# Performance work log

Measured on AMD Instinct MI355X. Metric: run time of the kernel, lower is better.

Reference implementation:

```python
import jax, jax.numpy as jnp
import numpy as np

NGRAMS = 5


def _pair_idx():
    pairs = [(i, j) for i in range(NGRAMS) for j in range(i + 1, NGRAMS)]
    return (np.array([p[0] for p in pairs]), np.array([p[1] for p in pairs]))


def setup_inputs() -> dict:
    key = jax.random.key(0)
    ks = jax.random.split(key, 12)
    B, S, U = 8, 500, 128
    n = NGRAMS
    C = S // n          # 100 chunks
    F = n * (n - 1)     # 2 * C(n,2) = 20 edge-concat feature width
    H, DK = n, 2        # per-chunk MHA: 5 heads, key_dim=value_dim=2
    GH, GD = 4, U // 4  # graph MHA: 4 heads, key_dim=32
    s = 0.05
    inp = {
        'x': jax.random.normal(ks[0], (B, S, U), jnp.float32),
        'wq': s * jax.random.normal(ks[1], (C, F, H, DK), jnp.float32),
        'bq': jnp.zeros((C, H, DK), jnp.float32),
        'wk': s * jax.random.normal(ks[2], (C, F, H, DK), jnp.float32),
        'bk': jnp.zeros((C, H, DK), jnp.float32),
        'wv': s * jax.random.normal(ks[3], (C, F, H, DK), jnp.float32),
        'bv': jnp.zeros((C, H, DK), jnp.float32),
        'wo': s * jax.random.normal(ks[4], (C, H, DK, F), jnp.float32),
        'bo': jnp.zeros((C, F), jnp.float32),
        'pos': 0.02 * jax.random.normal(ks[5], (C, U), jnp.float32),
        'gwq': s * jax.random.normal(ks[6], (U, GH, GD), jnp.float32),
        'gbq': jnp.zeros((GH, GD), jnp.float32),
        'gwk': s * jax.random.normal(ks[7], (U, GH, GD), jnp.float32),
        'gbk': jnp.zeros((GH, GD), jnp.float32),
        'gwv': s * jax.random.normal(ks[8], (U, GH, GD), jnp.float32),
        'gbv': jnp.zeros((GH, GD), jnp.float32),
        'gwo': s * jax.random.normal(ks[9], (GH, GD, U), jnp.float32),
        'gbo': jnp.zeros((U,), jnp.float32),
    }
    return inp


def reference(x, wq, bq, wk, bk, wv, bv, wo, bo, pos,
              gwq, gbq, gwk, gbk, gwv, gbv, gwo, gbo):
    B, S, U = x.shape
    n = NGRAMS
    C = S // n
    ii, jj = _pair_idx()
    P = ii.shape[0]
    # [B,S,U] -> [B,U,S] -> chunks [B,U,C,n]
    xt = jnp.transpose(x, (0, 2, 1)).reshape(B, U, C, n)
    # edge construction: concat of every node pair per chunk -> [B,U,C,2P]
    H_edges = jnp.stack([xt[..., ii], xt[..., jj]], axis=-1).reshape(B, U, C, 2 * P)
    Ht = jnp.transpose(H_edges, (0, 2, 1, 3))  # [B,C,U,F], attention seq axis = U
    dk = wq.shape[-1]
    scale = 1.0 / jnp.sqrt(jnp.asarray(dk, x.dtype))
    q = (jnp.einsum('bcuf,cfhd->bcuhd', Ht, wq) + bq[None, :, None]) * scale
    k = jnp.einsum('bcuf,cfhd->bcuhd', Ht, wk) + bk[None, :, None]
    v = jnp.einsum('bcuf,cfhd->bcuhd', Ht, wv) + bv[None, :, None]
    scores = jnp.einsum('bcuhd,bcvhd->bchuv', q, k)
    attn = jax.nn.softmax(scores, axis=-1)
    o = jnp.einsum('bchuv,bcvhd->bcuhd', attn, v)
    mha_out = jnp.einsum('bcuhd,chdf->bcuf', o, wo) + bo[None, :, None]
    alpha = jax.nn.leaky_relu(Ht + mha_out, negative_slope=0.3)  # [B,C,U,F]
    # stack + reduce_mean over edge-feature axis, transpose -> [B,C,U]
    g = jnp.mean(alpha, axis=-1)
    g = g + pos[None]  # learned position embedding over C
    # graph-level self-attention over the C axis
    gdk = gwq.shape[-1]
    gscale = 1.0 / jnp.sqrt(jnp.asarray(gdk, x.dtype))
    gq = (jnp.einsum('bcu,uhd->bchd', g, gwq) + gbq) * gscale
    gk = jnp.einsum('bcu,uhd->bchd', g, gwk) + gbk
    gv = jnp.einsum('bcu,uhd->bchd', g, gwv) + gbv
    gs = jnp.einsum('bqhd,bkhd->bhqk', gq, gk)
    ga = jax.nn.softmax(gs, axis=-1)
    go = jnp.einsum('bhqk,bkhd->bqhd', ga, gv)
    g_attn = jnp.einsum('bqhd,hdu->bqu', go, gwo) + gbo
    return g + g_attn  # [B, C, U]
```

## Files before the change

kernel.cpp:

```cpp
#include <hip/hip_runtime.h>

#define NB  8
#define SS  500
#define UU  128
#define NG  5
#define CC  100
#define PP  10
#define FF  20
#define HH  5
#define HD  10
#define GHH 4
#define GDD 32

__global__ __launch_bounds__(128) void k1_chunk_mha(
    const float* __restrict__ x,   const float* __restrict__ wq,
    const float* __restrict__ bq,  const float* __restrict__ wk,
    const float* __restrict__ bk,  const float* __restrict__ wv,
    const float* __restrict__ bv,  const float* __restrict__ wo,
    const float* __restrict__ bo,  const float* __restrict__ pos,
    const float* __restrict__ gwq, const float* __restrict__ gbq,
    const float* __restrict__ gwk, const float* __restrict__ gbk,
    const float* __restrict__ gwv, const float* __restrict__ gbv,
    float* __restrict__ g_out, float* __restrict__ gq_out,
    float* __restrict__ gk_out, float* __restrict__ gv_out)
{
    const int bc = blockIdx.x;
    const int b  = bc / CC, c = bc % CC;
    const int u  = threadIdx.x;

    __shared__ float4 s_kv[UU][HH];
    __shared__ float  s_g[UU];

    float xv[NG];
    const float* xb = x + (size_t)b * SS * UU + (size_t)c * NG * UU + u;
#pragma unroll
    for (int t = 0; t < NG; ++t) xv[t] = xb[t * UU];

    const int II[PP] = {0,0,0,0,1,1,1,2,2,3};
    const int JJ[PP] = {1,2,3,4,2,3,4,3,4,4};
    float ht[FF];
#pragma unroll
    for (int p = 0; p < PP; ++p) { ht[2*p] = xv[II[p]]; ht[2*p+1] = xv[JJ[p]]; }

    const float* wqc = wq + c * (FF * HD);
    const float* wkc = wk + c * (FF * HD);
    const float* wvc = wv + c * (FF * HD);
    float qv[HD], kv[HD], vv[HD];
#pragma unroll
    for (int hd = 0; hd < HD; ++hd) {
        qv[hd] = bq[c*HD + hd]; kv[hd] = bk[c*HD + hd]; vv[hd] = bv[c*HD + hd];
    }
#pragma unroll
    for (int f = 0; f < FF; ++f) {
        const float hf = ht[f];
#pragma unroll
        for (int hd = 0; hd < HD; ++hd) {
            qv[hd] = fmaf(hf, wqc[f*HD + hd], qv[hd]);
            kv[hd] = fmaf(hf, wkc[f*HD + hd], kv[hd]);
            vv[hd] = fmaf(hf, wvc[f*HD + hd], vv[hd]);
        }
    }
#pragma unroll
    for (int h = 0; h < HH; ++h)
        s_kv[u][h] = make_float4(kv[2*h], kv[2*h+1], vv[2*h], vv[2*h+1]);
    __syncthreads();

    const float scale = 0.7071067811865476f;
    float q0[HH], q1[HH], l[HH], o0[HH], o1[HH];
#pragma unroll
    for (int h = 0; h < HH; ++h) {
        q0[h] = qv[2*h] * scale; q1[h] = qv[2*h+1] * scale;
        l[h] = 0.f; o0[h] = 0.f; o1[h] = 0.f;
    }
#pragma unroll 2
    for (int vi = 0; vi < UU; ++vi) {
#pragma unroll
        for (int h = 0; h < HH; ++h) {
            const float4 kvv = s_kv[vi][h];
            const float s = fmaf(q0[h], kvv.x, q1[h] * kvv.y);
            const float e = __expf(s);
            l[h]  += e;
            o0[h]  = fmaf(e, kvv.z, o0[h]);
            o1[h]  = fmaf(e, kvv.w, o1[h]);
        }
    }
    float o[HD];
#pragma unroll
    for (int h = 0; h < HH; ++h) {
        const float inv = 1.f / l[h];
        o[2*h] = o0[h] * inv; o[2*h+1] = o1[h] * inv;
    }

    const float* woc = wo + c * (HD * FF);
    float gsum = 0.f;
#pragma unroll
    for (int f = 0; f < FF; ++f) {
        float acc = bo[c*FF + f];
#pragma unroll
        for (int hd = 0; hd < HD; ++hd) acc = fmaf(o[hd], woc[hd*FF + f], acc);
        const float a = ht[f] + acc;
        gsum += (a > 0.f) ? a : 0.3f * a;
    }
    const float g = gsum * (1.f / FF) + pos[c*UU + u];
    g_out[(size_t)bc*UU + u] = g;
    s_g[u] = g;
    __syncthreads();

    const float gscale = 0.17677669529663687f;
    float aq = gbq[u], ak = gbk[u], av = gbv[u];
    for (int u2 = 0; u2 < UU; ++u2) {
        const float gu = s_g[u2];
        aq = fmaf(gu, gwq[u2*UU + u], aq);
        ak = fmaf(gu, gwk[u2*UU + u], ak);
        av = fmaf(gu, gwv[u2*UU + u], av);
    }
    gq_out[(size_t)bc*UU + u] = aq * gscale;
    gk_out[(size_t)bc*UU + u] = ak;
    gv_out[(size_t)bc*UU + u] = av;
}

__global__ __launch_bounds__(128) void k2_graph_attn(
    const float* gq, const float* __restrict__ gk,
    const float* __restrict__ gv, float* go)
{
    const int b = blockIdx.x / GHH, h = blockIdx.x % GHH;
    const int t = threadIdx.x;
    __shared__ float4 s_k[CC][GDD/4], s_v[CC][GDD/4];

    const float4* gk4 = (const float4*)(gk + (size_t)b * CC * UU);
    const float4* gv4 = (const float4*)(gv + (size_t)b * CC * UU);
    for (int idx = t; idx < CC * 8; idx += 128) {
        const int k = idx >> 3, d4 = idx & 7;
        s_k[k][d4] = gk4[k*32 + h*8 + d4];
        s_v[k][d4] = gv4[k*32 + h*8 + d4];
    }
    float4 qf[8];
    if (t < CC) {
        const float4* q4 = (const float4*)(gq + (size_t)b*CC*UU + (size_t)t*UU + h*GDD);
#pragma unroll
        for (int i = 0; i < 8; ++i) qf[i] = q4[i];
    }
    __syncthreads();

    if (t < CC) {
        float l = 0.f;
        float4 o[8];
#pragma unroll
        for (int i = 0; i < 8; ++i) o[i] = make_float4(0.f, 0.f, 0.f, 0.f);
        for (int k = 0; k < CC; ++k) {
            float s = 0.f;
#pragma unroll
            for (int i = 0; i < 8; ++i) {
                const float4 kf = s_k[k][i];
                s = fmaf(qf[i].x, kf.x, s); s = fmaf(qf[i].y, kf.y, s);
                s = fmaf(qf[i].z, kf.z, s); s = fmaf(qf[i].w, kf.w, s);
            }
            const float e = __expf(s);
            l += e;
#pragma unroll
            for (int i = 0; i < 8; ++i) {
                const float4 vf = s_v[k][i];
                o[i].x = fmaf(e, vf.x, o[i].x); o[i].y = fmaf(e, vf.y, o[i].y);
                o[i].z = fmaf(e, vf.z, o[i].z); o[i].w = fmaf(e, vf.w, o[i].w);
            }
        }
        const float inv = 1.f / l;
        float4* go4 = (float4*)(go + (size_t)b*CC*UU + (size_t)t*UU + h*GDD);
#pragma unroll
        for (int i = 0; i < 8; ++i) {
            o[i].x *= inv; o[i].y *= inv; o[i].z *= inv; o[i].w *= inv;
            go4[i] = o[i];
        }
    }
}

__global__ __launch_bounds__(128) void k3_out(
    const float* __restrict__ go, const float* __restrict__ gwo,
    const float* __restrict__ gbo, float* out)
{
    const int bq = blockIdx.x;
    const int u  = threadIdx.x;
    __shared__ float s_go[UU];
    s_go[u] = go[(size_t)bq*UU + u];
    __syncthreads();
    float acc = gbo[u];
    for (int hd = 0; hd < UU; ++hd)
        acc = fmaf(s_go[hd], gwo[hd*UU + u], acc);
    out[(size_t)bq*UU + u] += acc;
}

extern "C" void kernel_launch(void* const* d_in, const int* in_sizes, int n_in,
                              void* d_out, int out_size, void* d_ws, size_t ws_size,
                              hipStream_t stream)
{
    (void)in_sizes; (void)n_in; (void)out_size; (void)ws_size;
    const float* x   = (const float*)d_in[0];
    const float* wq  = (const float*)d_in[1];
    const float* bq  = (const float*)d_in[2];
    const float* wk  = (const float*)d_in[3];
    const float* bk  = (const float*)d_in[4];
    const float* wv  = (const float*)d_in[5];
    const float* bv  = (const float*)d_in[6];
    const float* wo  = (const float*)d_in[7];
    const float* bo  = (const float*)d_in[8];
    const float* pos = (const float*)d_in[9];
    const float* gwq = (const float*)d_in[10];
    const float* gbq = (const float*)d_in[11];
    const float* gwk = (const float*)d_in[12];
    const float* gbk = (const float*)d_in[13];
    const float* gwv = (const float*)d_in[14];
    const float* gbv = (const float*)d_in[15];
    const float* gwo = (const float*)d_in[16];
    const float* gbo = (const float*)d_in[17];
    float* out = (float*)d_out;
    float* ws  = (float*)d_ws;

    float* gq_ws = ws;
    float* gk_ws = ws + 102400;
    float* gv_ws = ws + 204800;

    k1_chunk_mha<<<NB*CC, 128, 0, stream>>>(x, wq, bq, wk, bk, wv, bv, wo, bo,
        pos, gwq, gbq, gwk, gbk, gwv, gbv, out, gq_ws, gk_ws, gv_ws);
    k2_graph_attn<<<NB*GHH, 128, 0, stream>>>(gq_ws, gk_ws, gv_ws, gq_ws);
    k3_out<<<NB*CC, 128, 0, stream>>>(gq_ws, gwo, gbo, out);
}
```

Measured before the change: 145.9 us.

## Split chunk MHA across heads and fuse graph attention with output projection

The chunk kernel now runs 640 threads per block, one group of 128 per head, instead of one thread looping over all five heads. The per-chunk projection and graph QKV work is split across these groups and combined with shared-memory reductions. The graph attention and output projection kernels merge into one kernel with a block per (batch, query). That block recomputes scores over all keys and reads V straight from global memory. This adds parallelism to the serial softmax loop and the small k2 grid, and removes one launch, at the cost of extra syncs and repeated K/V reads per query.

```diff
diff --git a/kernel.cpp b/kernel.cpp
--- a/kernel.cpp
+++ b/kernel.cpp
@@ -12,7 +12,7 @@
 #define GHH 4
 #define GDD 32
 
-__global__ __launch_bounds__(128) void k1_chunk_mha(
+__global__ __launch_bounds__(640) void k1_chunk_mha(
     const float* __restrict__ x,   const float* __restrict__ wq,
     const float* __restrict__ bq,  const float* __restrict__ wk,
     const float* __restrict__ bk,  const float* __restrict__ wv,
@@ -26,10 +26,14 @@
 {
     const int bc = blockIdx.x;
     const int b  = bc / CC, c = bc % CC;
-    const int u  = threadIdx.x;
+    const int u  = threadIdx.x & 127;
+    const int h  = threadIdx.x >> 7;
 
     __shared__ float4 s_kv[UU][HH];
+    __shared__ float2 s_o[UU][HH];
+    __shared__ float  s_part[HH][UU];
     __shared__ float  s_g[UU];
+    __shared__ float  s_red[3][HH][UU];
 
     float xv[NG];
     const float* xb = x + (size_t)b * SS * UU + (size_t)c * NG * UU + u;
@@ -42,151 +46,144 @@
 #pragma unroll
     for (int p = 0; p < PP; ++p) { ht[2*p] = xv[II[p]]; ht[2*p+1] = xv[JJ[p]]; }
 
-    const float* wqc = wq + c * (FF * HD);
-    const float* wkc = wk + c * (FF * HD);
-    const float* wvc = wv + c * (FF * HD);
-    float qv[HD], kv[HD], vv[HD];
-#pragma unroll
-    for (int hd = 0; hd < HD; ++hd) {
-        qv[hd] = bq[c*HD + hd]; kv[hd] = bk[c*HD + hd]; vv[hd] = bv[c*HD + hd];
-    }
+    const int cb = c * (FF * HD) + 2 * h;
+    float q0 = bq[c*HD + 2*h], q1 = bq[c*HD + 2*h + 1];
+    float k0 = bk[c*HD + 2*h], k1 = bk[c*HD + 2*h + 1];
+    float v0 = bv[c*HD + 2*h], v1 = bv[c*HD + 2*h + 1];
 #pragma unroll
     for (int f = 0; f < FF; ++f) {
         const float hf = ht[f];
-#pragma unroll
-        for (int hd = 0; hd < HD; ++hd) {
-            qv[hd] = fmaf(hf, wqc[f*HD + hd], qv[hd]);
-            kv[hd] = fmaf(hf, wkc[f*HD + hd], kv[hd]);
-            vv[hd] = fmaf(hf, wvc[f*HD + hd], vv[hd]);
-        }
-    }
-#pragma unroll
-    for (int h = 0; h < HH; ++h)
-        s_kv[u][h] = make_float4(kv[2*h], kv[2*h+1], vv[2*h], vv[2*h+1]);
+        q0 = fmaf(hf, wq[cb + f*HD],     q0);
+        q1 = fmaf(hf, wq[cb + f*HD + 1], q1);
+        k0 = fmaf(hf, wk[cb + f*HD],     k0);
+        k1 = fmaf(hf, wk[cb + f*HD + 1], k1);
+        v0 = fmaf(hf, wv[cb + f*HD],     v0);
+        v1 = fmaf(hf, wv[cb + f*HD + 1], v1);
+    }
+    s_kv[u][h] = make_float4(k0, k1, v0, v1);
     __syncthreads();
 
     const float scale = 0.7071067811865476f;
-    float q0[HH], q1[HH], l[HH], o0[HH], o1[HH];
-#pragma unroll
-    for (int h = 0; h < HH; ++h) {
-        q0[h] = qv[2*h] * scale; q1[h] = qv[2*h+1] * scale;
-        l[h] = 0.f; o0[h] = 0.f; o1[h] = 0.f;
-    }
-#pragma unroll 2
+    q0 *= scale; q1 *= scale;
+    float l = 0.f, o0 = 0.f, o1 = 0.f;
+#pragma unroll 4
     for (int vi = 0; vi < UU; ++vi) {
-#pragma unroll
-        for (int h = 0; h < HH; ++h) {
-            const float4 kvv = s_kv[vi][h];
-            const float s = fmaf(q0[h], kvv.x, q1[h] * kvv.y);
-            const float e = __expf(s);
-            l[h]  += e;
-            o0[h]  = fmaf(e, kvv.z, o0[h]);
-            o1[h]  = fmaf(e, kvv.w, o1[h]);
-        }
-    }
-    float o[HD];
-#pragma unroll
-    for (int h = 0; h < HH; ++h) {
-        const float inv = 1.f / l[h];
-        o[2*h] = o0[h] * inv; o[2*h+1] = o1[h] * inv;
-    }
-
+        const float4 kvv = s_kv[vi][h];
+        const float s = fmaf(q0, kvv.x, q1 * kvv.y);
+        const float e = __expf(s);
+        l += e;
+        o0 = fmaf(e, kvv.z, o0);
+        o1 = fmaf(e, kvv.w, o1);
+    }
+    const float inv = 1.f / l;
+    s_o[u][h] = make_float2(o0 * inv, o1 * inv);
+    __syncthreads();
+
+    float ov[HD];
+#pragma unroll
+    for (int h2 = 0; h2 < HH; ++h2) {
+        const float2 t2 = s_o[u][h2];
+        ov[2*h2] = t2.x; ov[2*h2+1] = t2.y;
+    }
     const float* woc = wo + c * (HD * FF);
-    float gsum = 0.f;
-#pragma unroll
-    for (int f = 0; f < FF; ++f) {
+    float part = 0.f;
+#pragma unroll
+    for (int j = 0; j < 4; ++j) {
+        const int f = h * 4 + j;
         float acc = bo[c*FF + f];
 #pragma unroll
-        for (int hd = 0; hd < HD; ++hd) acc = fmaf(o[hd], woc[hd*FF + f], acc);
+        for (int hd = 0; hd < HD; ++hd) acc = fmaf(ov[hd], woc[hd*FF + f], acc);
         const float a = ht[f] + acc;
-        gsum += (a > 0.f) ? a : 0.3f * a;
-    }
-    const float g = gsum * (1.f / FF) + pos[c*UU + u];
-    g_out[(size_t)bc*UU + u] = g;
-    s_g[u] = g;
-    __syncthreads();
-
-    const float gscale = 0.17677669529663687f;
-    float aq = gbq[u], ak = gbk[u], av = gbv[u];
-    for (int u2 = 0; u2 < UU; ++u2) {
+        part += (a > 0.f) ? a : 0.3f * a;
+    }
+    s_part[h][u] = part;
+    __syncthreads();
+
+    if (h == 0) {
+        const float gsum = s_part[0][u] + s_part[1][u] + s_part[2][u]
+                         + s_part[3][u] + s_part[4][u];
+        const float g = gsum * (1.f / FF) + pos[c*UU + u];
+        s_g[u] = g;
+        g_out[(size_t)bc*UU + u] = g;
+    }
+    __syncthreads();
+
+    const int st = h * 26, en = (h == 4) ? UU : st + 26;
+    float aq = (h == 0) ? gbq[u] : 0.f;
+    float ak = (h == 0) ? gbk[u] : 0.f;
+    float av = (h == 0) ? gbv[u] : 0.f;
+    for (int u2 = st; u2 < en; ++u2) {
         const float gu = s_g[u2];
         aq = fmaf(gu, gwq[u2*UU + u], aq);
         ak = fmaf(gu, gwk[u2*UU + u], ak);
         av = fmaf(gu, gwv[u2*UU + u], av);
     }
-    gq_out[(size_t)bc*UU + u] = aq * gscale;
-    gk_out[(size_t)bc*UU + u] = ak;
-    gv_out[(size_t)bc*UU + u] = av;
+    s_red[0][h][u] = aq; s_red[1][h][u] = ak; s_red[2][h][u] = av;
+    __syncthreads();
+
+    if (h < 3) {
+        const float sum = s_red[h][0][u] + s_red[h][1][u] + s_red[h][2][u]
+                        + s_red[h][3][u] + s_red[h][4][u];
+        if (h == 0)      gq_out[(size_t)bc*UU + u] = sum * 0.17677669529663687f;
+        else if (h == 1) gk_out[(size_t)bc*UU + u] = sum;
+        else             gv_out[(size_t)bc*UU + u] = sum;
+    }
 }
 
-__global__ __launch_bounds__(128) void k2_graph_attn(
-    const float* gq, const float* __restrict__ gk,
-    const float* __restrict__ gv, float* go)
-{
-    const int b = blockIdx.x / GHH, h = blockIdx.x % GHH;
-    const int t = threadIdx.x;
-    __shared__ float4 s_k[CC][GDD/4], s_v[CC][GDD/4];
-
-    const float4* gk4 = (const float4*)(gk + (size_t)b * CC * UU);
-    const float4* gv4 = (const float4*)(gv + (size_t)b * CC * UU);
-    for (int idx = t; idx < CC * 8; idx += 128) {
-        const int k = idx >> 3, d4 = idx & 7;
-        s_k[k][d4] = gk4[k*32 + h*8 + d4];
-        s_v[k][d4] = gv4[k*32 + h*8 + d4];
-    }
-    float4 qf[8];
-    if (t < CC) {
-        const float4* q4 = (const float4*)(gq + (size_t)b*CC*UU + (size_t)t*UU + h*GDD);
-#pragma unroll
-        for (int i = 0; i < 8; ++i) qf[i] = q4[i];
-    }
-    __syncthreads();
-
-    if (t < CC) {
-        float l = 0.f;
-        float4 o[8];
-#pragma unroll
-        for (int i = 0; i < 8; ++i) o[i] = make_float4(0.f, 0.f, 0.f, 0.f);
-        for (int k = 0; k < CC; ++k) {
-            float s = 0.f;
-#pragma unroll
-            for (int i = 0; i < 8; ++i) {
-                const float4 kf = s_k[k][i];
-                s = fmaf(qf[i].x, kf.x, s); s = fmaf(qf[i].y, kf.y, s);
-                s = fmaf(qf[i].z, kf.z, s); s = fmaf(qf[i].w, kf.w, s);
-            }
-            const float e = __expf(s);
-            l += e;
-#pragma unroll
-            for (int i = 0; i < 8; ++i) {
-                const float4 vf = s_v[k][i];
-                o[i].x = fmaf(e, vf.x, o[i].x); o[i].y = fmaf(e, vf.y, o[i].y);
-                o[i].z = fmaf(e, vf.z, o[i].z); o[i].w = fmaf(e, vf.w, o[i].w);
-            }
-        }
-        const float inv = 1.f / l;
-        float4* go4 = (float4*)(go + (size_t)b*CC*UU + (size_t)t*UU + h*GDD);
-#pragma unroll
-        for (int i = 0; i < 8; ++i) {
-            o[i].x *= inv; o[i].y *= inv; o[i].z *= inv; o[i].w *= inv;
-            go4[i] = o[i];
-        }
-    }
-}
-
-__global__ __launch_bounds__(128) void k3_out(
-    const float* __restrict__ go, const float* __restrict__ gwo,
-    const float* __restrict__ gbo, float* out)
+__global__ __launch_bounds__(128) void k2_graph(
+    const float* __restrict__ gq, const float* __restrict__ gk,
+    const float* __restrict__ gv, const float* __restrict__ gwo,
+    const float* __restrict__ gbo, float* __restrict__ out)
 {
     const int bq = blockIdx.x;
-    const int u  = threadIdx.x;
-    __shared__ float s_go[UU];
-    s_go[u] = go[(size_t)bq*UU + u];
-    __syncthreads();
-    float acc = gbo[u];
+    const int b  = bq / CC;
+    const int t  = threadIdx.x;
+
+    __shared__ float s_q[UU];
+    __shared__ float s_e[GHH][CC];
+    __shared__ float s_o[UU];
+
+    const float gval = out[(size_t)bq*UU + t];
+    s_q[t] = gq[(size_t)bq*UU + t];
+    __syncthreads();
+
+    if (t < CC) {
+        const float4* krow = (const float4*)(gk + ((size_t)b*CC + t)*UU);
+        const float4* q4   = (const float4*)s_q;
+#pragma unroll
+        for (int hh = 0; hh < GHH; ++hh) {
+            float s = 0.f;
+#pragma unroll
+            for (int i = 0; i < 8; ++i) {
+                const float4 kf = krow[hh*8 + i];
+                const float4 qf = q4[hh*8 + i];
+                s = fmaf(qf.x, kf.x, s); s = fmaf(qf.y, kf.y, s);
+                s = fmaf(qf.z, kf.z, s); s = fmaf(qf.w, kf.w, s);
+            }
+            s_e[hh][t] = __expf(s);
+        }
+    }
+    __syncthreads();
+
+    {
+        const int h = t >> 5;
+        const float* vcol = gv + (size_t)b*CC*UU + t;
+        float l = 0.f, o = 0.f;
+#pragma unroll 4
+        for (int k = 0; k < CC; ++k) {
+            const float e = s_e[h][k];
+            l += e;
+            o = fmaf(e, vcol[(size_t)k*UU], o);
+        }
+        s_o[t] = o / l;
+    }
+    __syncthreads();
+
+    float acc = gbo[t];
+#pragma unroll 4
     for (int hd = 0; hd < UU; ++hd)
-        acc = fmaf(s_go[hd], gwo[hd*UU + u], acc);
-    out[(size_t)bq*UU + u] += acc;
+        acc = fmaf(s_o[hd], gwo[hd*UU + t], acc);
+    out[(size_t)bq*UU + t] = gval + acc;
 }
 
 extern "C" void kernel_launch(void* const* d_in, const int* in_sizes, int n_in,
@@ -219,8 +216,7 @@
     float* gk_ws = ws + 102400;
     float* gv_ws = ws + 204800;
 
-    k1_chunk_mha<<<NB*CC, 128, 0, stream>>>(x, wq, bq, wk, bk, wv, bv, wo, bo,
+    k1_chunk_mha<<<NB*CC, 640, 0, stream>>>(x, wq, bq, wk, bk, wv, bv, wo, bo,
         pos, gwq, gbq, gwk, gbk, gwv, gbv, out, gq_ws, gk_ws, gv_ws);
-    k2_graph_attn<<<NB*GHH, 128, 0, stream>>>(gq_ws, gk_ws, gv_ws, gq_ws);
-    k3_out<<<NB*CC, 128, 0, stream>>>(gq_ws, gwo, gbo, out);
+    k2_graph<<<NB*CC, 128, 0, stream>>>(gq_ws, gk_ws, gv_ws, gwo, gbo, out);
 }
```

New measurement: 156.3 us. 7.2% more time.
